# Kernel optimization log

Hardware: AMD Instinct MI355X
Metric: run time of the kernel (lower is better)

## Reference

```python
import jax, jax.numpy as jnp
import numpy as np

NEG_SLOPE = 0.01  # F.leaky_relu default


def _unfold3(x):
    # x: [B,C,H,W] -> [B,C,9,H,W] of 3x3 neighborhoods (zero pad 1)
    B, C, H, W = x.shape
    xp = jnp.pad(x, ((0, 0), (0, 0), (1, 1), (1, 1)))
    return jnp.stack([xp[:, :, i:i + H, j:j + W] for i in range(3) for j in range(3)], axis=2)


def _resize_bilinear(img, oh, ow):
    # torch F.interpolate mode='bilinear', align_corners=False, antialias=False
    B, C, H, W = img.shape
    if oh == H and ow == W:
        return img
    def coords(out, inn):
        c = jnp.maximum((jnp.arange(out, dtype=jnp.float32) + 0.5) * (inn / out) - 0.5, 0.0)
        i0 = jnp.floor(c).astype(jnp.int32)
        i1 = jnp.minimum(i0 + 1, inn - 1)
        w = c - i0.astype(jnp.float32)
        return i0, i1, w
    i0, i1, wh = coords(oh, H)
    row = img[:, :, i0, :] * (1.0 - wh)[None, None, :, None] + img[:, :, i1, :] * wh[None, None, :, None]
    j0, j1, ww = coords(ow, W)
    return row[:, :, :, j0] * (1.0 - ww) + row[:, :, :, j1] * ww


def _up2_nearest(x):
    # F.interpolate scale_factor=2 (default mode='nearest')
    return jnp.repeat(jnp.repeat(x, 2, axis=2), 2, axis=3)


def _leaky(x):
    return jnp.where(x >= 0, x, NEG_SLOPE * x)


def _pac_conv(x, guide, w):
    # PacConv2d (gaussian kernel, k=3, stride=1, pad=1, bias=False)
    g_unf = _unfold3(guide)                      # [B,Cg,9,H,W]
    diff = g_unf - guide[:, :, None]             # f_j - f_i
    kern = jnp.exp(-0.5 * jnp.sum(diff * diff, axis=1))  # [B,9,H,W]
    x_unf = _unfold3(x)                          # [B,Ci,9,H,W]
    wk = w.reshape(w.shape[0], w.shape[1], 9)    # [Co,Ci,9]
    return jnp.einsum('oik,bikhw,bkhw->bohw', wk, x_unf, kern)


def setup_inputs() -> dict:
    key = jax.random.key(0)
    ks = jax.random.split(key, 8)
    B, Cx, Hx, Wx = 4, 384, 32, 32
    Hg = Wg = 512
    x = jax.random.normal(ks[0], (B, Cx, Hx, Wx), dtype=jnp.float32)
    guide = jax.random.uniform(ks[1], (B, 3, Hg, Wg), dtype=jnp.float32)
    lin_w = jax.random.normal(ks[2], (16, 384, 1, 1), dtype=jnp.float32) * 0.05
    lin_b = jax.random.normal(ks[3], (16,), dtype=jnp.float32) * 0.05
    chans = [16, 4, 4, 4, 1]
    w0 = jax.random.normal(ks[4], (chans[1], chans[0], 3, 3), dtype=jnp.float32) * 0.1
    w1 = jax.random.normal(ks[5], (chans[2], chans[1], 3, 3), dtype=jnp.float32) * 0.1
    w2 = jax.random.normal(ks[6], (chans[3], chans[2], 3, 3), dtype=jnp.float32) * 0.1
    w3 = jax.random.normal(ks[7], (chans[4], chans[3], 3, 3), dtype=jnp.float32) * 0.1
    return {"x": x, "guide": guide, "lin_w": lin_w, "lin_b": lin_b,
            "w0": w0, "w1": w1, "w2": w2, "w3": w3}


def reference(x, guide, lin_w, lin_b, w0, w1, w2, w3):
    # crop guide to multiple of 16 (module uses shape[-1] for both dims)
    s = (guide.shape[-1] // 16) * 16
    guide = guide[..., :s, :s]
    # 1x1 conv + leaky relu
    x = jnp.einsum('oi,bihw->bohw', lin_w[:, :, 0, 0], x) + lin_b[None, :, None, None]
    x = _leaky(x)
    ws = [w0, w1, w2, w3]
    n = len(ws)
    Hg, Wg = guide.shape[2], guide.shape[3]
    for i in range(n):
        f = 2 ** (n - 1 - i)
        g = _resize_bilinear(guide, Hg // f, Wg // f)
        x = _up2_nearest(x)
        x = _pac_conv(x, g, ws[i])
        if i < n - 1:
            x = _leaky(x)
    return jax.nn.sigmoid(x)
```

## Files before the change

kernel.cpp:

```cpp
#include <hip/hip_runtime.h>
#include <math.h>

#define NEG_SLOPE 0.01f

__device__ inline float bilin(const float* __restrict__ gp, float scale, int r, int c) {
    float ch = fmaxf((r + 0.5f) * scale - 0.5f, 0.f);
    float cw = fmaxf((c + 0.5f) * scale - 0.5f, 0.f);
    int h0 = (int)ch, w0 = (int)cw;
    int h1 = min(h0 + 1, 511), w1 = min(w0 + 1, 511);
    float fh = ch - (float)h0, fw = cw - (float)w0;
    float v00 = gp[h0 * 512 + w0], v01 = gp[h0 * 512 + w1];
    float v10 = gp[h1 * 512 + w0], v11 = gp[h1 * 512 + w1];
    float top = v00 + (v01 - v00) * fw;
    float bot = v10 + (v11 - v10) * fw;
    return top + (bot - top) * fh;
}

__global__ void __launch_bounds__(256)
prep_kernel(const float* __restrict__ x, const float* __restrict__ lw,
            const float* __restrict__ lb, float* __restrict__ x16,
            const float* __restrict__ g, float* __restrict__ g64p,
            float* __restrict__ g128p, float* __restrict__ g256p) {
    int bid = blockIdx.x;
    if (bid < 256) {
        int idx = bid * 256 + threadIdx.x;
        int hw = idx & 1023, co = (idx >> 10) & 15, bb = idx >> 14;
        const float* xp = x + bb * 384 * 1024 + hw;
        const float* wp = lw + co * 384;
        float a0 = 0.f, a1 = 0.f, a2 = 0.f, a3 = 0.f;
        for (int ci = 0; ci < 384; ci += 4) {
            a0 = fmaf(wp[ci],     xp[(ci)     * 1024], a0);
            a1 = fmaf(wp[ci + 1], xp[(ci + 1) * 1024], a1);
            a2 = fmaf(wp[ci + 2], xp[(ci + 2) * 1024], a2);
            a3 = fmaf(wp[ci + 3], xp[(ci + 3) * 1024], a3);
        }
        float acc = lb[co] + ((a0 + a1) + (a2 + a3));
        x16[idx] = acc >= 0.f ? acc : NEG_SLOPE * acc;
    } else {
        int idx = (bid - 256) * 256 + threadIdx.x;
        int R; float scale; float* outp; int o;
        if (idx < 786432)      { R = 256; scale = 2.f; outp = g256p; o = idx; }
        else if (idx < 983040) { R = 128; scale = 4.f; outp = g128p; o = idx - 786432; }
        else                   { R = 64;  scale = 8.f; outp = g64p;  o = idx - 983040; }
        int c = o % R;
        int r = (o / R) % R;
        int bc = o / (R * R);
        outp[o] = bilin(g + (size_t)bc * 262144, scale, r, c);
    }
}

template <int Ci, int Co, int R, int ACT>
__global__ void __launch_bounds__(256)
pac_stage(const float* __restrict__ x, const float* __restrict__ g,
          const float* __restrict__ wk, float* __restrict__ out) {
    __shared__ float sw[Co * Ci * 9];
    for (int i = threadIdx.x; i < Co * Ci * 9; i += 256) sw[i] = wk[i];
    __syncthreads();

    constexpr int HW = R * R;
    constexpr int Rh = R / 2;
    constexpr int HWh = Rh * Rh;
    int idx = blockIdx.x * 256 + threadIdx.x;
    int w = idx & (R - 1);
    int h = (idx / R) & (R - 1);
    int b = idx / HW;

    const float* gb = g + (size_t)b * 3 * HW;
    int ctr = h * R + w;
    float gc0 = gb[ctr];
    float gc1 = gb[HW + ctr];
    float gc2 = gb[2 * HW + ctr];

    float acc[Co];
#pragma unroll
    for (int co = 0; co < Co; ++co) acc[co] = 0.f;

    const float* xb = x + (size_t)b * Ci * HWh;

#pragma unroll
    for (int t = 0; t < 9; ++t) {
        int dh = t / 3 - 1, dw = t % 3 - 1;
        int hh = h + dh, ww = w + dw;
        if (hh < 0 || hh >= R || ww < 0 || ww >= R) continue;
        int tap = hh * R + ww;
        float d0 = gb[tap] - gc0;
        float d1 = gb[HW + tap] - gc1;
        float d2 = gb[2 * HW + tap] - gc2;
        float k = __expf(-0.5f * (d0 * d0 + d1 * d1 + d2 * d2));
        const float* xp = xb + (hh >> 1) * Rh + (ww >> 1);
#pragma unroll
        for (int ci = 0; ci < Ci; ++ci) {
            float xv = xp[ci * HWh] * k;
#pragma unroll
            for (int co = 0; co < Co; ++co)
                acc[co] = fmaf(sw[(co * Ci + ci) * 9 + t], xv, acc[co]);
        }
    }

#pragma unroll
    for (int co = 0; co < Co; ++co) {
        float v = acc[co];
        if (ACT == 0) v = v >= 0.f ? v : NEG_SLOPE * v;
        else          v = 1.0f / (1.0f + __expf(-v));
        out[(size_t)(b * Co + co) * HW + ctr] = v;
    }
}

extern "C" void kernel_launch(void* const* d_in, const int* in_sizes, int n_in,
                              void* d_out, int out_size, void* d_ws, size_t ws_size,
                              hipStream_t stream) {
    const float* x     = (const float*)d_in[0];
    const float* guide = (const float*)d_in[1];
    const float* lin_w = (const float*)d_in[2];
    const float* lin_b = (const float*)d_in[3];
    const float* w0    = (const float*)d_in[4];
    const float* w1    = (const float*)d_in[5];
    const float* w2    = (const float*)d_in[6];
    const float* w3    = (const float*)d_in[7];
    float* out = (float*)d_out;

    float* ws    = (float*)d_ws;
    float* x16   = ws;
    float* g64p  = x16 + 65536;
    float* g128p = g64p + 49152;
    float* g256p = g128p + 196608;
    float* x0    = g256p + 786432;
    float* x1    = x0 + 65536;
    float* x2    = x1 + 262144;

    prep_kernel<<<4288, 256, 0, stream>>>(x, lin_w, lin_b, x16, guide, g64p, g128p, g256p);
    pac_stage<16, 4, 64, 0><<<64, 256, 0, stream>>>(x16, g64p, w0, x0);
    pac_stage<4, 4, 128, 0><<<256, 256, 0, stream>>>(x0, g128p, w1, x1);
    pac_stage<4, 4, 256, 0><<<1024, 256, 0, stream>>>(x1, g256p, w2, x2);
    pac_stage<4, 1, 512, 1><<<4096, 256, 0, stream>>>(x2, guide, w3, out);
}
```

Measured before the change: 125.5 us.

## Fuse last two PAC stages into one tiled kernel with LDS halos

Replaces the separate 256- and 512-resolution PAC launches with one kernel. Each block loads a 32x32 output tile's guide, downsampled guide and stage-1 activations (with halos) into shared memory, computes the 18x18 intermediate stage-2 tile in LDS, then produces the final sigmoid output. This removes the global write and read of the 256x256 intermediate and one launch, at the cost of recomputing halo pixels and lower occupancy from the shared-memory footprint. The block index mapping groups blocks of the same batch onto the same XCD.

```diff
diff --git a/kernel.cpp b/kernel.cpp
--- a/kernel.cpp
+++ b/kernel.cpp
@@ -106,6 +106,132 @@
     }
 }
 
+template <int Ci, int Co>
+__device__ inline void pac_lds(const float* __restrict__ sx, int BXr, int BXc, int NX,
+                               const float* __restrict__ sg, int BGr, int BGc, int NG,
+                               const float* __restrict__ sw, float* __restrict__ so,
+                               int BOr, int BOc, int NO, int RES) {
+    const int NG2 = NG * NG, NX2 = NX * NX, NO2 = NO * NO;
+    for (int i = threadIdx.x; i < NO2; i += 256) {
+        int r = i / NO, c = i % NO;
+        int gh = BOr + r, gw = BOc + c;
+        float acc[Co];
+#pragma unroll
+        for (int co = 0; co < Co; ++co) acc[co] = 0.f;
+        if (gh >= 0 && gh < RES && gw >= 0 && gw < RES) {
+            int lc0 = (gh - BGr) * NG + (gw - BGc);
+            float gc0 = sg[lc0], gc1 = sg[NG2 + lc0], gc2 = sg[2 * NG2 + lc0];
+#pragma unroll
+            for (int tt = 0; tt < 9; ++tt) {
+                int hh = gh + tt / 3 - 1, ww = gw + tt % 3 - 1;
+                if (hh < 0 || hh >= RES || ww < 0 || ww >= RES) continue;
+                int lt = (hh - BGr) * NG + (ww - BGc);
+                float d0 = sg[lt] - gc0;
+                float d1 = sg[NG2 + lt] - gc1;
+                float d2 = sg[2 * NG2 + lt] - gc2;
+                float k = __expf(-0.5f * (d0 * d0 + d1 * d1 + d2 * d2));
+                int lx = ((hh >> 1) - BXr) * NX + ((ww >> 1) - BXc);
+#pragma unroll
+                for (int ci = 0; ci < Ci; ++ci) {
+                    float xv = sx[ci * NX2 + lx] * k;
+#pragma unroll
+                    for (int co = 0; co < Co; ++co)
+                        acc[co] = fmaf(sw[(co * Ci + ci) * 9 + tt], xv, acc[co]);
+                }
+            }
+        }
+#pragma unroll
+        for (int co = 0; co < Co; ++co) {
+            float v = acc[co];
+            so[co * NO2 + i] = v >= 0.f ? v : NEG_SLOPE * v;
+        }
+    }
+}
+
+__global__ void __launch_bounds__(256)
+pac_tail_kernel(const float* __restrict__ x1g, const float* __restrict__ guide,
+                const float* __restrict__ g256p,
+                const float* __restrict__ w2, const float* __restrict__ w3,
+                float* __restrict__ out) {
+    __shared__ float smem[6544];
+    float* sw2   = smem;
+    float* sw3   = smem + 144;
+    float* sg512 = smem + 180;
+    float* sg256 = smem + 3648;
+    float* sx1   = smem + 4848;
+    float* sx2   = smem + 5248;
+
+    int bid = blockIdx.x;
+    int xcd = bid & 7;
+    int j   = bid >> 3;
+    int b    = xcd >> 1;
+    int half = xcd & 1;
+    int t = half * 8 + (j >> 4);
+    int u = j & 15;
+
+    const int B1r = 8 * t - 1,   B1c = 8 * u - 1;
+    const int BG2r = 16 * t - 2, BG2c = 16 * u - 2;
+    const int B2r = 16 * t - 1,  B2c = 16 * u - 1;
+    const int BG3r = 32 * t - 1, BG3c = 32 * u - 1;
+
+    const float* gb = guide + (size_t)b * 3 * 262144;
+
+    for (int i = threadIdx.x; i < 3468; i += 256) {
+        int ch = i / 1156, rem = i % 1156, r = rem / 34, c = rem % 34;
+        int gr = BG3r + r, gc = BG3c + c;
+        float v = 0.f;
+        if (gr >= 0 && gr < 512 && gc >= 0 && gc < 512)
+            v = gb[ch * 262144 + (gr << 9) + gc];
+        sg512[i] = v;
+    }
+    for (int i = threadIdx.x; i < 1200; i += 256) {
+        int ch = i / 400, rem = i % 400, r = rem / 20, c = rem % 20;
+        int gr = BG2r + r, gc = BG2c + c;
+        float v = 0.f;
+        if (gr >= 0 && gr < 256 && gc >= 0 && gc < 256)
+            v = g256p[(b * 3 + ch) * 65536 + (gr << 8) + gc];
+        sg256[i] = v;
+    }
+    for (int i = threadIdx.x; i < 400; i += 256) {
+        int ci = i / 100, rem = i % 100, r = rem / 10, c = rem % 10;
+        int gr = B1r + r, gc = B1c + c;
+        float v = 0.f;
+        if (gr >= 0 && gr < 128 && gc >= 0 && gc < 128)
+            v = x1g[((b * 4 + ci) << 14) + (gr << 7) + gc];
+        sx1[i] = v;
+    }
+    for (int i = threadIdx.x; i < 144; i += 256) sw2[i] = w2[i];
+    for (int i = threadIdx.x; i < 36;  i += 256) sw3[i] = w3[i];
+    __syncthreads();
+
+    pac_lds<4, 4>(sx1, B1r, B1c, 10, sg256, BG2r, BG2c, 20, sw2, sx2, B2r, B2c, 18, 256);
+    __syncthreads();
+
+    float* ob = out + (size_t)b * 262144;
+    for (int i = threadIdx.x; i < 1024; i += 256) {
+        int r = i >> 5, c = i & 31;
+        int gh = 32 * t + r, gw = 32 * u + c;
+        int lc0 = (gh - BG3r) * 34 + (gw - BG3c);
+        float gc0 = sg512[lc0], gc1 = sg512[1156 + lc0], gc2 = sg512[2 * 1156 + lc0];
+        float acc = 0.f;
+#pragma unroll
+        for (int tt = 0; tt < 9; ++tt) {
+            int hh = gh + tt / 3 - 1, ww = gw + tt % 3 - 1;
+            if (hh < 0 || hh >= 512 || ww < 0 || ww >= 512) continue;
+            int lt = (hh - BG3r) * 34 + (ww - BG3c);
+            float d0 = sg512[lt] - gc0;
+            float d1 = sg512[1156 + lt] - gc1;
+            float d2 = sg512[2 * 1156 + lt] - gc2;
+            float k = __expf(-0.5f * (d0 * d0 + d1 * d1 + d2 * d2));
+            int lx = ((hh >> 1) - B2r) * 18 + ((ww >> 1) - B2c);
+#pragma unroll
+            for (int ci = 0; ci < 4; ++ci)
+                acc = fmaf(sw3[ci * 9 + tt], sx2[ci * 324 + lx] * k, acc);
+        }
+        ob[(gh << 9) + gw] = 1.0f / (1.0f + __expf(-acc));
+    }
+}
+
 extern "C" void kernel_launch(void* const* d_in, const int* in_sizes, int n_in,
                               void* d_out, int out_size, void* d_ws, size_t ws_size,
                               hipStream_t stream) {
@@ -126,11 +252,9 @@
     float* g256p = g128p + 196608;
     float* x0    = g256p + 786432;
     float* x1    = x0 + 65536;
-    float* x2    = x1 + 262144;
 
     prep_kernel<<<4288, 256, 0, stream>>>(x, lin_w, lin_b, x16, guide, g64p, g128p, g256p);
     pac_stage<16, 4, 64, 0><<<64, 256, 0, stream>>>(x16, g64p, w0, x0);
     pac_stage<4, 4, 128, 0><<<256, 256, 0, stream>>>(x0, g128p, w1, x1);
-    pac_stage<4, 4, 256, 0><<<1024, 256, 0, stream>>>(x1, g256p, w2, x2);
-    pac_stage<4, 1, 512, 1><<<4096, 256, 0, stream>>>(x2, guide, w3, out);
-}
+    pac_tail_kernel<<<1024, 256, 0, stream>>>(x1, guide, g256p, w2, w3, out);
+}
```

Measured after the change: 134.7 us. 7.3% more time.
